# Kernel optimization log

Hardware: AMD Instinct MI355X
Metric: run time of the kernel (lower is better)

The kernel has to match this reference:

```python
import jax, jax.numpy as jnp
import numpy as np

S, B, P, E = 2048, 128, 1024, 192  # seq len, batch, single_eval_pos, embedding_size
NAN_IND, INF_IND, NEG_INF_IND = -2.0, 2.0, 4.0


def setup_inputs() -> dict:
    key = jax.random.key(0)
    k1, k2, k3 = jax.random.split(key, 3)
    y = jax.random.normal(k1, (S, B, 1), jnp.float32)
    # nn.Linear(in_features=2, out_features=E): weight [E, 2], bias [E]
    W = jax.random.normal(k2, (E, 2), jnp.float32) * 0.1
    b = jax.random.normal(k3, (E,), jnp.float32) * 0.1
    return {"y": y, "W": W, "b": b, "single_eval_pos": P}


def reference(y, W, b, single_eval_pos):
    sep = single_eval_pos
    # --- nan handling (nan_handling_y_encoder=True) ---
    prefix = y[:sep]                              # [P, B, 1]
    means = jnp.nanmean(prefix, axis=0)           # [B, 1] (torch.nanmean ignores NaN only)
    is_nan = jnp.isnan(y)
    is_inf = jnp.isinf(y)
    mask = is_nan | is_inf
    indicators = (is_nan * NAN_IND
                  + (is_inf & (y > 0)) * INF_IND
                  + (is_inf & (y < 0)) * NEG_INF_IND).astype(y.dtype)  # [S, B, 1]
    y_imp = jnp.where(mask, means[None], y)       # [S, B, 1]

    # --- multiclass rank encode (max_num_classes >= 2) ---
    # torch: rank[t,b] = #{distinct values v in train prefix of column b : v < y[t,b]}
    col = y_imp[..., 0]                           # [S, B]
    s = jnp.sort(col[:sep], axis=0)               # [P, B] sorted train prefix per batch
    # marker of first occurrence of each distinct value in the sorted prefix
    is_new = jnp.concatenate(
        [jnp.ones((1, s.shape[1]), bool), s[1:] != s[:-1]], axis=0)  # [P, B]
    # [S, P, B] boolean compare, masked to distinct values, reduce over P
    cmp = (col[:, None, :] > s[None, :, :]) & is_new[None]
    ranks = cmp.sum(axis=1).astype(y.dtype)[..., None]  # [S, B, 1]

    x = jnp.concatenate([ranks, indicators], axis=-1)   # [S, B, 2]
    return x @ W.T + b                                   # [S, B, E]
```

## Files before the change

### kernel.cpp

```cpp
#include <hip/hip_runtime.h>
#include <math.h>

#define S_DIM 2048
#define B_DIM 128
#define P_DIM 1024
#define E_DIM 192

__global__ __launch_bounds__(256) void prep_kernel(
    const float* __restrict__ y, const int* __restrict__ sep_p,
    float* __restrict__ u, int* __restrict__ Kout, float* __restrict__ meanout) {
  __shared__ float sm[P_DIM];
  __shared__ float redf[256];
  __shared__ int   redi[256];
  __shared__ int   scan[256];

  const int b   = blockIdx.x;
  const int tid = threadIdx.x;
  const int sep = *sep_p;

  float lsum = 0.f;
  int   lcnt = 0;
  for (int i = tid; i < P_DIM; i += 256) {
    float v = (i < sep) ? y[i * B_DIM + b] : INFINITY;
    sm[i] = v;
    if (i < sep && !isnan(v)) { lsum += v; lcnt++; }
  }
  redf[tid] = lsum;
  redi[tid] = lcnt;
  __syncthreads();
  for (int off = 128; off > 0; off >>= 1) {
    if (tid < off) { redf[tid] += redf[tid + off]; redi[tid] += redi[tid + off]; }
    __syncthreads();
  }
  const float mean = redf[0] / (float)redi[0];
  if (tid == 0) meanout[b] = mean;

  for (int i = tid; i < sep; i += 256) {
    float v = sm[i];
    if (isnan(v) || isinf(v)) sm[i] = mean;
  }
  __syncthreads();

  for (int k = 2; k <= P_DIM; k <<= 1) {
    for (int j = k >> 1; j > 0; j >>= 1) {
      for (int i = tid; i < P_DIM; i += 256) {
        int ixj = i ^ j;
        if (ixj > i) {
          float a = sm[i], c = sm[ixj];
          bool up = ((i & k) == 0);
          if (up ? (a > c) : (a < c)) { sm[i] = c; sm[ixj] = a; }
        }
      }
      __syncthreads();
    }
  }

  int flags[4];
  int lu = 0;
  for (int q = 0; q < 4; q++) {
    int i = tid * 4 + q;
    bool nw = (i == 0) || (sm[i] != sm[i - 1]);
    flags[q] = nw ? 1 : 0;
    lu += flags[q];
  }
  scan[tid] = lu;
  __syncthreads();
  for (int off = 1; off < 256; off <<= 1) {
    int t = (tid >= off) ? scan[tid - off] : 0;
    __syncthreads();
    scan[tid] += t;
    __syncthreads();
  }
  int excl = scan[tid] - lu;
  for (int q = 0; q < 4; q++) {
    int i = tid * 4 + q;
    if (flags[q]) { u[b * P_DIM + excl] = sm[i]; excl++; }
  }
  if (tid == 255) Kout[b] = scan[255];
}

__global__ __launch_bounds__(256) void rank_kernel(
    const float* __restrict__ y, const float* __restrict__ u,
    const int* __restrict__ Kv, const float* __restrict__ meanv,
    float2* __restrict__ ri) {
  __shared__ float su[P_DIM];
  const int b = blockIdx.x;
  const int K = Kv[b];
  const float mean = meanv[b];
  for (int i = threadIdx.x; i < K; i += 256) su[i] = u[b * P_DIM + i];
  __syncthreads();

  const int s = blockIdx.y * 256 + threadIdx.x;
  const float v = y[s * B_DIM + b];
  float ind = 0.f;
  float x = v;
  if (isnan(v))      { ind = -2.f; x = mean; }
  else if (isinf(v)) { ind = (v > 0.f) ? 2.f : 4.f; x = mean; }

  int lo = 0, hi = K;
  while (lo < hi) {
    int mid = (lo + hi) >> 1;
    if (su[mid] < x) lo = mid + 1; else hi = mid;
  }
  ri[b * S_DIM + s] = make_float2((float)lo, ind);
}

__global__ __launch_bounds__(256) void out_kernel(
    const float2* __restrict__ ri, const float4* __restrict__ Wf,
    const float4* __restrict__ bias4, float4* __restrict__ out, int total4) {
  const int stride = gridDim.x * blockDim.x;
  for (int idx = blockIdx.x * blockDim.x + threadIdx.x; idx < total4; idx += stride) {
    const int sb = idx / (E_DIM / 4);
    const int q  = idx - sb * (E_DIM / 4);
    const int s  = sb >> 7;
    const int b  = sb & (B_DIM - 1);
    const float2 r  = ri[b * S_DIM + s];
    const float4 wa = Wf[2 * q];
    const float4 wb = Wf[2 * q + 1];
    const float4 bb = bias4[q];
    float4 o;
    o.x = fmaf(r.x, wa.x, fmaf(r.y, wa.y, bb.x));
    o.y = fmaf(r.x, wa.z, fmaf(r.y, wa.w, bb.y));
    o.z = fmaf(r.x, wb.x, fmaf(r.y, wb.y, bb.z));
    o.w = fmaf(r.x, wb.z, fmaf(r.y, wb.w, bb.w));
    out[idx] = o;
  }
}

extern "C" void kernel_launch(void* const* d_in, const int* in_sizes, int n_in,
                              void* d_out, int out_size, void* d_ws, size_t ws_size,
                              hipStream_t stream) {
  const float* y    = (const float*)d_in[0];
  const float* W    = (const float*)d_in[1];
  const float* bias = (const float*)d_in[2];
  const int*   sep  = (const int*)d_in[3];

  char* ws = (char*)d_ws;
  float2* ri    = (float2*)ws;
  float*  u     = (float*)(ws + (size_t)S_DIM * B_DIM * sizeof(float2));
  int*    Kv    = (int*)(ws + (size_t)S_DIM * B_DIM * sizeof(float2)
                            + (size_t)B_DIM * P_DIM * sizeof(float));
  float*  meanv = (float*)((char*)Kv + 512);

  prep_kernel<<<B_DIM, 256, 0, stream>>>(y, sep, u, Kv, meanv);

  dim3 g2(B_DIM, S_DIM / 256);
  rank_kernel<<<g2, 256, 0, stream>>>(y, u, Kv, meanv, ri);

  const int total4 = S_DIM * B_DIM * (E_DIM / 4);
  out_kernel<<<2048, 256, 0, stream>>>(ri, (const float4*)W, (const float4*)bias,
                                       (float4*)d_out, total4);
}
```

Measured before the change: 241.5 us.

## Fuse prep and rank kernels, restructure output kernel with hoisted weights and nontemporal stores

```diff
diff --git a/kernel.cpp b/kernel.cpp
--- a/kernel.cpp
+++ b/kernel.cpp
@@ -5,14 +5,20 @@
 #define B_DIM 128
 #define P_DIM 1024
 #define E_DIM 192
+#define SB    (S_DIM * B_DIM)
 
-__global__ __launch_bounds__(256) void prep_kernel(
+typedef float f32x4 __attribute__((ext_vector_type(4)));
+typedef float f32x2 __attribute__((ext_vector_type(2)));
+
+__global__ __launch_bounds__(256) void prep_rank_kernel(
     const float* __restrict__ y, const int* __restrict__ sep_p,
-    float* __restrict__ u, int* __restrict__ Kout, float* __restrict__ meanout) {
+    f32x2* __restrict__ ri) {
   __shared__ float sm[P_DIM];
+  __shared__ float su[P_DIM];
   __shared__ float redf[256];
   __shared__ int   redi[256];
   __shared__ int   scan[256];
+  __shared__ int   Ksh;
 
   const int b   = blockIdx.x;
   const int tid = threadIdx.x;
@@ -33,7 +39,6 @@
     __syncthreads();
   }
   const float mean = redf[0] / (float)redi[0];
-  if (tid == 0) meanout[b] = mean;
 
   for (int i = tid; i < sep; i += 256) {
     float v = sm[i];
@@ -74,56 +79,48 @@
   int excl = scan[tid] - lu;
   for (int q = 0; q < 4; q++) {
     int i = tid * 4 + q;
-    if (flags[q]) { u[b * P_DIM + excl] = sm[i]; excl++; }
+    if (flags[q]) { su[excl] = sm[i]; excl++; }
   }
-  if (tid == 255) Kout[b] = scan[255];
+  if (tid == 255) Ksh = scan[255];
+  __syncthreads();
+
+  const int K = Ksh;
+
+  for (int s = tid; s < S_DIM; s += 256) {
+    const float v = y[s * B_DIM + b];
+    float ind = 0.f;
+    float x = v;
+    if (isnan(v))      { ind = -2.f; x = mean; }
+    else if (isinf(v)) { ind = (v > 0.f) ? 2.f : 4.f; x = mean; }
+    int lo = 0, hi = K;
+    while (lo < hi) {
+      int mid = (lo + hi) >> 1;
+      if (su[mid] < x) lo = mid + 1; else hi = mid;
+    }
+    f32x2 rv; rv.x = (float)lo; rv.y = ind;
+    ri[b * S_DIM + s] = rv;
+  }
 }
 
-__global__ __launch_bounds__(256) void rank_kernel(
-    const float* __restrict__ y, const float* __restrict__ u,
-    const int* __restrict__ Kv, const float* __restrict__ meanv,
-    float2* __restrict__ ri) {
-  __shared__ float su[P_DIM];
-  const int b = blockIdx.x;
-  const int K = Kv[b];
-  const float mean = meanv[b];
-  for (int i = threadIdx.x; i < K; i += 256) su[i] = u[b * P_DIM + i];
-  __syncthreads();
-
-  const int s = blockIdx.y * 256 + threadIdx.x;
-  const float v = y[s * B_DIM + b];
-  float ind = 0.f;
-  float x = v;
-  if (isnan(v))      { ind = -2.f; x = mean; }
-  else if (isinf(v)) { ind = (v > 0.f) ? 2.f : 4.f; x = mean; }
-
-  int lo = 0, hi = K;
-  while (lo < hi) {
-    int mid = (lo + hi) >> 1;
-    if (su[mid] < x) lo = mid + 1; else hi = mid;
-  }
-  ri[b * S_DIM + s] = make_float2((float)lo, ind);
-}
-
-__global__ __launch_bounds__(256) void out_kernel(
-    const float2* __restrict__ ri, const float4* __restrict__ Wf,
-    const float4* __restrict__ bias4, float4* __restrict__ out, int total4) {
-  const int stride = gridDim.x * blockDim.x;
-  for (int idx = blockIdx.x * blockDim.x + threadIdx.x; idx < total4; idx += stride) {
-    const int sb = idx / (E_DIM / 4);
-    const int q  = idx - sb * (E_DIM / 4);
-    const int s  = sb >> 7;
-    const int b  = sb & (B_DIM - 1);
-    const float2 r  = ri[b * S_DIM + s];
-    const float4 wa = Wf[2 * q];
-    const float4 wb = Wf[2 * q + 1];
-    const float4 bb = bias4[q];
-    float4 o;
-    o.x = fmaf(r.x, wa.x, fmaf(r.y, wa.y, bb.x));
-    o.y = fmaf(r.x, wa.z, fmaf(r.y, wa.w, bb.y));
-    o.z = fmaf(r.x, wb.x, fmaf(r.y, wb.y, bb.z));
-    o.w = fmaf(r.x, wb.z, fmaf(r.y, wb.w, bb.w));
-    out[idx] = o;
+__global__ __launch_bounds__(192) void out_kernel(
+    const f32x2* __restrict__ ri, const f32x4* __restrict__ Wf,
+    const f32x4* __restrict__ bias4, f32x4* __restrict__ out) {
+  const int q  = threadIdx.x % 48;
+  const int r0 = threadIdx.x / 48;
+  const f32x4 wa = Wf[2 * q];
+  const f32x4 wb = Wf[2 * q + 1];
+  const f32x4 bb = bias4[q];
+  const int stride = gridDim.x * 4;
+  for (int sb = blockIdx.x * 4 + r0; sb < SB; sb += stride) {
+    const int s = sb >> 7;
+    const int b = sb & (B_DIM - 1);
+    const f32x2 rv = ri[b * S_DIM + s];
+    f32x4 o;
+    o.x = fmaf(rv.x, wa.x, fmaf(rv.y, wa.y, bb.x));
+    o.y = fmaf(rv.x, wa.z, fmaf(rv.y, wa.w, bb.y));
+    o.z = fmaf(rv.x, wb.x, fmaf(rv.y, wb.y, bb.z));
+    o.w = fmaf(rv.x, wb.z, fmaf(rv.y, wb.w, bb.w));
+    __builtin_nontemporal_store(o, &out[(size_t)sb * 48 + q]);
   }
 }
 
@@ -135,19 +132,10 @@
   const float* bias = (const float*)d_in[2];
   const int*   sep  = (const int*)d_in[3];
 
-  char* ws = (char*)d_ws;
-  float2* ri    = (float2*)ws;
-  float*  u     = (float*)(ws + (size_t)S_DIM * B_DIM * sizeof(float2));
-  int*    Kv    = (int*)(ws + (size_t)S_DIM * B_DIM * sizeof(float2)
-                            + (size_t)B_DIM * P_DIM * sizeof(float));
-  float*  meanv = (float*)((char*)Kv + 512);
+  f32x2* ri = (f32x2*)d_ws;
 
-  prep_kernel<<<B_DIM, 256, 0, stream>>>(y, sep, u, Kv, meanv);
+  prep_rank_kernel<<<B_DIM, 256, 0, stream>>>(y, sep, ri);
 
-  dim3 g2(B_DIM, S_DIM / 256);
-  rank_kernel<<<g2, 256, 0, stream>>>(y, u, Kv, meanv, ri);
-
-  const int total4 = S_DIM * B_DIM * (E_DIM / 4);
-  out_kernel<<<2048, 256, 0, stream>>>(ri, (const float4*)W, (const float4*)bias,
-                                       (float4*)d_out, total4);
+  out_kernel<<<4096, 192, 0, stream>>>(ri, (const f32x4*)W,
+                                       (const f32x4*)bias, (f32x4*)d_out);
 }
```

Result: slower. 253.4 us (+4.9%).
